# Optimization experiments

Hardware: AMD Instinct MI355X
Metric: run time of the kernel (lower is better)

The kernel has to match this reference:

```python
import jax, jax.numpy as jnp
import numpy as np

D_MODEL = 1024
NUM_HEADS = 16
HEAD_DIM = D_MODEL // NUM_HEADS
FF_DIM = 4096
EPS = 1e-5


def _layer_norm(x, gamma, beta):
    mu = jnp.mean(x, axis=-1, keepdims=True)
    var = jnp.var(x, axis=-1, keepdims=True)
    return (x - mu) * jax.lax.rsqrt(var + EPS) * gamma + beta


def setup_inputs() -> dict:
    key0 = jax.random.key(0)
    ks = jax.random.split(key0, 20)
    s = 0.02
    B, S = 2, 2048
    inp = {
        'value': jax.random.normal(ks[0], (B, S, D_MODEL), jnp.float32),
        'key': jax.random.normal(ks[1], (B, S, D_MODEL), jnp.float32),
        'query': jax.random.normal(ks[2], (B, S, D_MODEL), jnp.float32),
        # attention projections (stored [in, out]; y = x @ W + b)
        'wq': jax.random.normal(ks[3], (D_MODEL, D_MODEL), jnp.float32) * s,
        'bq': jnp.zeros((D_MODEL,), jnp.float32),
        'wk': jax.random.normal(ks[4], (D_MODEL, D_MODEL), jnp.float32) * s,
        'bk': jnp.zeros((D_MODEL,), jnp.float32),
        'wv': jax.random.normal(ks[5], (D_MODEL, D_MODEL), jnp.float32) * s,
        'bv': jnp.zeros((D_MODEL,), jnp.float32),
        'wo': jax.random.normal(ks[6], (D_MODEL, D_MODEL), jnp.float32) * s,
        'bo': jnp.zeros((D_MODEL,), jnp.float32),
        # layernorm 1
        'g1': jnp.ones((D_MODEL,), jnp.float32),
        'beta1': jnp.zeros((D_MODEL,), jnp.float32),
        # feed-forward
        'w1': jax.random.normal(ks[7], (D_MODEL, FF_DIM), jnp.float32) * s,
        'b1': jnp.zeros((FF_DIM,), jnp.float32),
        'w2': jax.random.normal(ks[8], (FF_DIM, D_MODEL), jnp.float32) * s,
        'b2': jnp.zeros((D_MODEL,), jnp.float32),
        # layernorm 2
        'g2': jnp.ones((D_MODEL,), jnp.float32),
        'beta2': jnp.zeros((D_MODEL,), jnp.float32),
    }
    return inp


def reference(value, key, query, wq, bq, wk, bk, wv, bv, wo, bo,
              g1, beta1, w1, b1, w2, b2, g2, beta2):
    B, S, _ = query.shape
    # QKV projections -> [B, S, H, Dh]
    Q = (query @ wq + bq).reshape(B, S, NUM_HEADS, HEAD_DIM)
    K = (key @ wk + bk).reshape(B, S, NUM_HEADS, HEAD_DIM)
    V = (value @ wv + bv).reshape(B, S, NUM_HEADS, HEAD_DIM)
    # scaled dot-product attention (full score matrix, as in source)
    energy = jnp.einsum('bqhd,bkhd->bhqk', Q, K) / jnp.sqrt(jnp.float32(HEAD_DIM))
    attn = jax.nn.softmax(energy, axis=-1)
    out = jnp.einsum('bhqk,bkhd->bqhd', attn, V).reshape(B, S, D_MODEL)
    attn_out = out @ wo + bo
    # residual + norm1 (dropout is identity in eval)
    x = _layer_norm(attn_out + query, g1, beta1)
    # feed-forward
    ff = jax.nn.relu(x @ w1 + b1) @ w2 + b2
    # residual + norm2
    return _layer_norm(ff + x, g2, beta2)
```

## Files before the change

kernel.cpp:

```cpp
#include <hip/hip_runtime.h>
#include <hip/hip_bf16.h>
#include <cstdint>
#include <math.h>

typedef __bf16 bf16_t;
typedef __attribute__((ext_vector_type(2))) __bf16 bf16x2;
typedef __attribute__((ext_vector_type(4))) __bf16 bf16x4;
typedef __attribute__((ext_vector_type(8))) __bf16 bf16x8;
typedef __attribute__((ext_vector_type(4))) float f32x4;
typedef __attribute__((ext_vector_type(16))) float f32x16;
typedef __attribute__((ext_vector_type(2))) int int2v;
typedef __attribute__((ext_vector_type(4))) int int4v;

#define B_SZ 2
#define S_SZ 2048
#define D_MODEL 1024
#define NUM_HEADS 16
#define HEAD_DIM 64
#define FF_DIM 4096
#define M_ROWS (B_SZ * S_SZ)

#define CF 0.180336880f
#define THRC 2.0f

__device__ __forceinline__ float fexp2(float x) { return __builtin_amdgcn_exp2f(x); }

__device__ __forceinline__ void gload_lds16(const void* g, void* lds) {
    __builtin_amdgcn_global_load_lds(
        (const __attribute__((address_space(1))) void*)(uintptr_t)g,
        (__attribute__((address_space(3))) void*)(uint32_t)(uintptr_t)lds,
        16, 0, 0);
}

__device__ __forceinline__ f32x4 mfma16(bf16x8 a, bf16x8 b, f32x4 c) {
    return __builtin_amdgcn_mfma_f32_16x16x32_bf16(a, b, c, 0, 0, 0);
}
__device__ __forceinline__ f32x16 mfma32(bf16x8 a, bf16x8 b, f32x16 c) {
    return __builtin_amdgcn_mfma_f32_32x32x16_bf16(a, b, c, 0, 0, 0);
}
__device__ __forceinline__ int2v plswap(int a, int b) {
    return __builtin_amdgcn_permlane32_swap(a, b, false, false);
}
__device__ __forceinline__ int packbf(float a, float b) {
    bf16x2 t; t[0] = (bf16_t)a; t[1] = (bf16_t)b;
    return __builtin_bit_cast(int, t);
}

__device__ __forceinline__ int xcd_swz(int lin, int nwg) {
    return (lin & 7) * (nwg >> 3) + (lin >> 3);
}

__global__ __launch_bounds__(256) void cast3_f32_bf16(const float* __restrict__ in0,
                                                      const float* __restrict__ in1,
                                                      const float* __restrict__ in2,
                                                      bf16_t* __restrict__ out0,
                                                      bf16_t* __restrict__ out1,
                                                      bf16_t* __restrict__ out2) {
    int which = blockIdx.x >> 12;
    int blk = blockIdx.x & 4095;
    const float* in = which == 0 ? in0 : which == 1 ? in1 : in2;
    bf16_t* out = which == 0 ? out0 : which == 1 ? out1 : out2;
    size_t i = ((size_t)blk * 256 + threadIdx.x) * 4;
    float4 v = *(const float4*)(in + i);
    bf16x4 o;
    o[0] = (bf16_t)v.x; o[1] = (bf16_t)v.y; o[2] = (bf16_t)v.z; o[3] = (bf16_t)v.w;
    *(bf16x4*)(out + i) = o;
}

__global__ __launch_bounds__(256) void transpose_cast_w4(const float* __restrict__ W0,
                                                         const float* __restrict__ W1,
                                                         const float* __restrict__ W2,
                                                         const float* __restrict__ W3,
                                                         bf16_t* __restrict__ T0,
                                                         bf16_t* __restrict__ T1,
                                                         bf16_t* __restrict__ T2,
                                                         bf16_t* __restrict__ T3) {
    __shared__ float t[32][33];
    const int K = 1024, N = 1024;
    const float* W = blockIdx.z == 0 ? W0 : blockIdx.z == 1 ? W1 : blockIdx.z == 2 ? W2 : W3;
    bf16_t* WT = blockIdx.z == 0 ? T0 : blockIdx.z == 1 ? T1 : blockIdx.z == 2 ? T2 : T3;
    int tid = threadIdx.x;
    int rr = tid >> 3, cc = (tid & 7) * 4;
    int k0 = blockIdx.x * 32, n0 = blockIdx.y * 32;
    float4 v = *(const float4*)(W + (size_t)(k0 + rr) * N + n0 + cc);
    t[rr][cc + 0] = v.x; t[rr][cc + 1] = v.y; t[rr][cc + 2] = v.z; t[rr][cc + 3] = v.w;
    __syncthreads();
    bf16x4 o;
    o[0] = (bf16_t)t[cc + 0][rr]; o[1] = (bf16_t)t[cc + 1][rr];
    o[2] = (bf16_t)t[cc + 2][rr]; o[3] = (bf16_t)t[cc + 3][rr];
    *(bf16x4*)(WT + (size_t)(n0 + rr) * K + k0 + cc) = o;
}

__global__ __launch_bounds__(256) void transpose_cast_w(const float* __restrict__ W,
                                                        bf16_t* __restrict__ WT,
                                                        int K, int N) {
    __shared__ float t[32][33];
    int tid = threadIdx.x;
    int rr = tid >> 3, cc = (tid & 7) * 4;
    int k0 = blockIdx.x * 32, n0 = blockIdx.y * 32;
    float4 v = *(const float4*)(W + (size_t)(k0 + rr) * N + n0 + cc);
    t[rr][cc + 0] = v.x; t[rr][cc + 1] = v.y; t[rr][cc + 2] = v.z; t[rr][cc + 3] = v.w;
    __syncthreads();
    bf16x4 o;
    o[0] = (bf16_t)t[cc + 0][rr]; o[1] = (bf16_t)t[cc + 1][rr];
    o[2] = (bf16_t)t[cc + 2][rr]; o[3] = (bf16_t)t[cc + 3][rr];
    *(bf16x4*)(WT + (size_t)(n0 + rr) * K + k0 + cc) = o;
}

__global__ __launch_bounds__(256) void transpose_v(const bf16_t* __restrict__ Vp,
                                                   bf16_t* __restrict__ VT) {
    __shared__ bf16_t t[32][34];
    int tid = threadIdx.x;
    int rr = tid >> 3, cc = (tid & 7) * 4;
    int bh = blockIdx.z;
    int b = bh >> 4, h = bh & 15;
    int s0 = blockIdx.x * 32, d0 = blockIdx.y * 32;
    bf16x4 v = *(const bf16x4*)(Vp + ((size_t)(b * S_SZ + s0 + rr)) * D_MODEL + h * HEAD_DIM + d0 + cc);
    t[rr][cc + 0] = v[0]; t[rr][cc + 1] = v[1]; t[rr][cc + 2] = v[2]; t[rr][cc + 3] = v[3];
    __syncthreads();
    bf16x4 o;
    o[0] = t[cc + 0][rr]; o[1] = t[cc + 1][rr]; o[2] = t[cc + 2][rr]; o[3] = t[cc + 3][rr];
    *(bf16x4*)(VT + ((size_t)(bh * HEAD_DIM + d0 + rr)) * S_SZ + s0 + cc) = o;
}

template<bool RELU, bool OUT_BF16, bool OUT_F32>
__device__ __forceinline__ void gemm_core(const bf16_t* __restrict__ A, int lda,
                                          const bf16_t* __restrict__ Bt, int ldb,
                                          const float* __restrict__ bias, bool useBias,
                                          float* __restrict__ Cf,
                                          bf16_t* __restrict__ Cb,
                                          int N, int Klen, int m0, int n0,
                                          bf16_t* sA, bf16_t* sB) {
    const int tid = threadIdx.x;
    const int lane = tid & 63, wave = tid >> 6;
    const int g = lane >> 4, r = lane & 15;
    const int wm = (wave >> 1) * 64, wn = (wave & 1) * 64;

    const bf16_t* Ablk = A + (size_t)m0 * lda;
    const bf16_t* Bblk = Bt + (size_t)n0 * ldb;
    const int c0 = wave * 64 + lane;
    const int c1 = c0 + 256;

    const bf16_t* a0 = Ablk + (size_t)(c0 >> 2) * lda + (c0 & 3) * 8;
    const bf16_t* a1 = Ablk + (size_t)(c1 >> 2) * lda + (c1 & 3) * 8;
    const bf16_t* b0 = Bblk + (size_t)(c0 >> 2) * ldb + (c0 & 3) * 8;
    const bf16_t* b1 = Bblk + (size_t)(c1 >> 2) * ldb + (c1 & 3) * 8;

    f32x4 acc[4][4];
#pragma unroll
    for (int i = 0; i < 4; i++)
#pragma unroll
        for (int j = 0; j < 4; j++)
#pragma unroll
            for (int e = 0; e < 4; e++) acc[i][j][e] = 0.f;

    auto stage = [&](int buf, int k0) {
        gload_lds16(a0 + k0, sA + buf * 4096 + wave * 512);
        gload_lds16(a1 + k0, sA + buf * 4096 + 2048 + wave * 512);
        gload_lds16(b0 + k0, sB + buf * 4096 + wave * 512);
        gload_lds16(b1 + k0, sB + buf * 4096 + 2048 + wave * 512);
    };
    auto compute = [&](int buf) {
        bf16x8 a[4], b[4];
#pragma unroll
        for (int i = 0; i < 4; i++)
            a[i] = *(const bf16x8*)(sA + buf * 4096 + (wm + i * 16 + r) * 32 + g * 8);
#pragma unroll
        for (int j = 0; j < 4; j++)
            b[j] = *(const bf16x8*)(sB + buf * 4096 + (wn + j * 16 + r) * 32 + g * 8);
#pragma unroll
        for (int i = 0; i < 4; i++)
#pragma unroll
            for (int j = 0; j < 4; j++)
                acc[i][j] = mfma16(a[i], b[j], acc[i][j]);
    };

    const int nk = Klen >> 5;
    stage(0, 0);
    stage(1, 32);
    int bc = 0, bs = 2;
    for (int s = 0; s < nk; ++s) {
        if (s + 2 < nk) {
            stage(bs, (s + 2) * 32);
            asm volatile("s_waitcnt vmcnt(8)" ::: "memory");
        } else if (s + 1 < nk) {
            asm volatile("s_waitcnt vmcnt(4)" ::: "memory");
        } else {
            asm volatile("s_waitcnt vmcnt(0)" ::: "memory");
        }
        __builtin_amdgcn_s_barrier();
        __builtin_amdgcn_sched_barrier(0);
        compute(bc);
        __builtin_amdgcn_sched_barrier(0);
        __builtin_amdgcn_s_barrier();
        bc = (bc + 1 == 3) ? 0 : bc + 1;
        bs = (bs + 1 == 3) ? 0 : bs + 1;
    }

#pragma unroll
    for (int j = 0; j < 4; j++) {
        int n = n0 + wn + j * 16 + r;
        float bv = useBias ? bias[n] : 0.f;
#pragma unroll
        for (int i = 0; i < 4; i++) {
#pragma unroll
            for (int rr = 0; rr < 4; rr++) {
                int mrow = m0 + wm + i * 16 + g * 4 + rr;
                float val = acc[i][j][rr] + bv;
                if (RELU) val = fmaxf(val, 0.f);
                if (OUT_F32) Cf[(size_t)mrow * N + n] = val;
                if (OUT_BF16) Cb[(size_t)mrow * N + n] = (bf16_t)val;
            }
        }
    }
}

template<bool RELU, bool OUT_BF16, bool OUT_F32>
__global__ __launch_bounds__(256) void gemm_bt(const bf16_t* __restrict__ A, int lda,
                                               const bf16_t* __restrict__ Bt, int ldb,
                                               const float* __restrict__ bias,
                                               float* __restrict__ Cf0,
                                               float* __restrict__ Cf1,
                                               bf16_t* __restrict__ Cb,
                                               int N, int Klen) {
    __shared__ bf16_t sA[3 * 4096];
    __shared__ bf16_t sB[3 * 4096];
    const int lin = blockIdx.x + gridDim.x * (blockIdx.y + gridDim.y * blockIdx.z);
    const int nwg = gridDim.x * gridDim.y * gridDim.z;
    const int swz = xcd_swz(lin, nwg);
    const int bx = swz % gridDim.x;
    const int rest = swz / gridDim.x;
    const int by = rest % gridDim.y;
    const int bz = rest / gridDim.y;
    const int koff = bz * Klen;
    gemm_core<RELU, OUT_BF16, OUT_F32>(A + koff, lda, Bt + koff, ldb, bias, bz == 0,
                                       bz ? Cf1 : Cf0, Cb, N, Klen, bx * 128, by * 128, sA, sB);
}

__global__ __launch_bounds__(256) void gemm_qkv(const bf16_t* __restrict__ A0,
                                                const bf16_t* __restrict__ A1,
                                                const bf16_t* __restrict__ A2,
                                                const bf16_t* __restrict__ B0,
                                                const bf16_t* __restrict__ B1,
                                                const bf16_t* __restrict__ B2,
                                                const float* __restrict__ b0,
                                                const float* __restrict__ b1,
                                                const float* __restrict__ b2,
                                                bf16_t* __restrict__ C0,
                                                bf16_t* __restrict__ C1,
                                                bf16_t* __restrict__ C2) {
    __shared__ bf16_t sA[3 * 4096];
    __shared__ bf16_t sB[3 * 4096];
    const int lin = blockIdx.x + gridDim.x * (blockIdx.y + gridDim.y * blockIdx.z);
    const int nwg = gridDim.x * gridDim.y * gridDim.z;
    const int swz = xcd_swz(lin, nwg);
    const int bx = swz % gridDim.x;
    const int rest = swz / gridDim.x;
    const int by = rest % gridDim.y;
    const int bz = rest / gridDim.y;
    const bf16_t* A = bz == 0 ? A0 : bz == 1 ? A1 : A2;
    const bf16_t* Bt = bz == 0 ? B0 : bz == 1 ? B1 : B2;
    const float* bias = bz == 0 ? b0 : bz == 1 ? b1 : b2;
    bf16_t* C = bz == 0 ? C0 : bz == 1 ? C1 : C2;
    gemm_core<false, true, false>(A, 1024, Bt, 1024, bias, true,
                                  nullptr, C, 1024, 1024, bx * 128, by * 128, sA, sB);
}

__device__ __forceinline__ void flash_tile(
    const char* kt, const char* vt, int l31, int hi,
    const bf16x8 (&bq)[4],
    f32x16& o0, f32x16& o1, float& mC, float& l_run)
{
    bf16x8 ak[4];
#pragma unroll
    for (int kb = 0; kb < 4; kb++)
        ak[kb] = *(const bf16x8*)(kt + l31 * 128 + (((kb << 1) | hi) ^ (l31 & 7)) * 16);
    bf16x8 av[4];
#pragma unroll
    for (int db = 0; db < 2; db++)
#pragma unroll
        for (int kb = 0; kb < 2; kb++)
            av[db * 2 + kb] = *(const bf16x8*)(vt + (db * 32 + l31) * 64 + ((((kb << 1) | hi)) ^ ((l31 >> 1) & 3)) * 16);

    f32x16 s;
#pragma unroll
    for (int e = 0; e < 16; e++) s[e] = 0.f;
#pragma unroll
    for (int kb = 0; kb < 4; kb++) s = mfma32(ak[kb], bq[kb], s);

    float ma = fmaxf(fmaxf(s[0], s[1]), fmaxf(s[2], s[3]));
    float mb = fmaxf(fmaxf(s[4], s[5]), fmaxf(s[6], s[7]));
    float mc = fmaxf(fmaxf(s[8], s[9]), fmaxf(s[10], s[11]));
    float md = fmaxf(fmaxf(s[12], s[13]), fmaxf(s[14], s[15]));
    float pmaxC = fmaxf(fmaxf(ma, mb), fmaxf(mc, md)) * CF;

    if (!__all(pmaxC <= mC + THRC)) {
        int2v pr = plswap(__float_as_int(pmaxC), __float_as_int(pmaxC));
        float rowmaxC = fmaxf(__int_as_float(pr[0]), __int_as_float(pr[1]));
        float mnewC = fmaxf(mC, rowmaxC);
        float alpha = fexp2(mC - mnewC);
        mC = mnewC;
        l_run *= alpha;
#pragma unroll
        for (int e = 0; e < 16; e++) { o0[e] *= alpha; o1[e] *= alpha; }
    }

#pragma unroll
    for (int e = 0; e < 16; e++) s[e] = fexp2(__builtin_fmaf(s[e], CF, -mC));
    float t0 = (s[0] + s[1]) + (s[2] + s[3]);
    float t1 = (s[4] + s[5]) + (s[6] + s[7]);
    float t2 = (s[8] + s[9]) + (s[10] + s[11]);
    float t3 = (s[12] + s[13]) + (s[14] + s[15]);
    l_run += (t0 + t1) + (t2 + t3);

#pragma unroll
    for (int kb2 = 0; kb2 < 2; kb2++) {
        const int bse = kb2 * 8;
        int W0 = packbf(s[bse + 0], s[bse + 1]);
        int W1 = packbf(s[bse + 2], s[bse + 3]);
        int W2 = packbf(s[bse + 4], s[bse + 5]);
        int W3 = packbf(s[bse + 6], s[bse + 7]);
        int2v r02 = plswap(W0, W2);
        int2v r13 = plswap(W1, W3);
        int4v fw; fw[0] = r02[0]; fw[1] = r13[0]; fw[2] = r02[1]; fw[3] = r13[1];
        bf16x8 pf = __builtin_bit_cast(bf16x8, fw);
        o0 = mfma32(av[kb2], pf, o0);
        o1 = mfma32(av[2 + kb2], pf, o1);
    }
}

__global__ __launch_bounds__(256) void flash_attn(const bf16_t* __restrict__ Qp,
                                                  const bf16_t* __restrict__ Kp,
                                                  const bf16_t* __restrict__ VT,
                                                  bf16_t* __restrict__ Oa) {
    __shared__ alignas(16) char lds[2][2][8192];
    const int tid = threadIdx.x;
    const int lane = tid & 63;
    const int wave = tid >> 6;
    const int half = wave >> 1;
    const int qt = wave & 1;
    const int l31 = lane & 31, hi = lane >> 5;

    const int lin = blockIdx.x + (blockIdx.y << 5) + (blockIdx.z << 9);
    const int swz = (lin & 7) * 128 + (lin >> 3);
    const int qb = swz & 31;
    const int h = (swz >> 5) & 15;
    const int b = swz >> 9;

    const int q0 = qb * 64 + qt * 32;

    const bf16_t* Qb = Qp + (size_t)b * S_SZ * D_MODEL + h * HEAD_DIM;
    const bf16_t* Kb = Kp + (size_t)b * S_SZ * D_MODEL + h * HEAD_DIM;
    const bf16_t* Vb = VT + ((size_t)(b * NUM_HEADS + h) * HEAD_DIM) * S_SZ;

    const int sh = wave & 1;
    const int skvbase = sh * (S_SZ / 2);
    const bool kRole = wave < 2;

    const bf16_t* src_run;
    size_t inner_stride;
    size_t tile_stride;
    char* dst0;
    char* dst1;
    if (kRole) {
        src_run = Kb + (size_t)(skvbase + (lane >> 3)) * D_MODEL + ((lane & 7) ^ (lane >> 3)) * 8;
        inner_stride = (size_t)8 * D_MODEL;
        tile_stride = (size_t)32 * D_MODEL;
        dst0 = &lds[0][sh][0] + lane * 16;
        dst1 = &lds[1][sh][0] + lane * 16;
    } else {
        src_run = Vb + (size_t)(lane >> 2) * S_SZ + skvbase + ((lane & 3) ^ ((lane >> 3) & 3)) * 8;
        inner_stride = (size_t)16 * S_SZ;
        tile_stride = 32;
        dst0 = &lds[0][sh][4096] + lane * 16;
        dst1 = &lds[1][sh][4096] + lane * 16;
    }

    bf16x8 bq[4];
#pragma unroll
    for (int kb = 0; kb < 4; kb++)
        bq[kb] = *(const bf16x8*)(Qb + (size_t)(q0 + l31) * D_MODEL + kb * 16 + hi * 8);

    f32x16 o0, o1;
#pragma unroll
    for (int e = 0; e < 16; e++) { o0[e] = 0.f; o1[e] = 0.f; }
    float mC = -1e30f, l_run = 0.f;

    const char* kt0 = &lds[0][half][0];
    const char* vt0 = &lds[0][half][4096];
    const char* kt1 = &lds[1][half][0];
    const char* vt1 = &lds[1][half][4096];

#pragma unroll
    for (int ii = 0; ii < 4; ii++)
        gload_lds16(src_run + ii * inner_stride, dst0 + ii * 1024);
    src_run += tile_stride;
    __syncthreads();

    for (int t = 0; t < 32; t += 2) {
#pragma unroll
        for (int ii = 0; ii < 4; ii++)
            gload_lds16(src_run + ii * inner_stride, dst1 + ii * 1024);
        src_run += tile_stride;
        flash_tile(kt0, vt0, l31, hi, bq, o0, o1, mC, l_run);
        __syncthreads();

        if (t + 2 < 32) {
#pragma unroll
            for (int ii = 0; ii < 4; ii++)
                gload_lds16(src_run + ii * inner_stride, dst0 + ii * 1024);
            src_run += tile_stride;
        }
        flash_tile(kt1, vt1, l31, hi, bq, o0, o1, mC, l_run);
        __syncthreads();
    }

    int2v lp = plswap(__float_as_int(l_run), __float_as_int(l_run));
    l_run = __int_as_float(lp[0]) + __int_as_float(lp[1]);

    float (*obuf)[2][64] = (float (*)[2][64])(&lds[0][0][0]);
    float (*mrg)[64][2] = (float (*)[64][2])(&lds[0][0][0] + 16384);
    if (half == 1) {
        mrg[qt][lane][0] = mC;
        mrg[qt][lane][1] = l_run;
#pragma unroll
        for (int e = 0; e < 16; e++) {
            obuf[e][qt][lane] = o0[e];
            obuf[16 + e][qt][lane] = o1[e];
        }
    }
    __syncthreads();
    if (half == 0) {
        const float m2C = mrg[qt][lane][0], l2 = mrg[qt][lane][1];
        const float mm = fmaxf(mC, m2C);
        const float e1 = fexp2(mC - mm);
        const float e2 = fexp2(m2C - mm);
        const float linv = 1.f / (l_run * e1 + l2 * e2);
        bf16_t* Orow = Oa + ((size_t)b * S_SZ + q0 + l31) * D_MODEL + h * HEAD_DIM;
#pragma unroll
        for (int db = 0; db < 2; db++) {
#pragma unroll
            for (int rq = 0; rq < 4; rq++) {
                bf16x4 st;
#pragma unroll
                for (int i = 0; i < 4; i++) {
                    const int e = rq * 4 + i;
                    const float own = db ? o1[e] : o0[e];
                    const float oth = obuf[db * 16 + e][qt][lane];
                    st[i] = (bf16_t)((own * e1 + oth * e2) * linv);
                }
                *(bf16x4*)(Orow + db * 32 + rq * 8 + hi * 4) = st;
            }
        }
    }
}

__global__ __launch_bounds__(256) void ln_fused(const float* __restrict__ A,
                                                const float* __restrict__ A2,
                                                const float* __restrict__ R,
                                                const float* __restrict__ gamma,
                                                const float* __restrict__ beta,
                                                float* __restrict__ Xf,
                                                bf16_t* __restrict__ Xb) {
    __shared__ float red[8];
    int row = blockIdx.x, tid = threadIdx.x;
    size_t base = (size_t)row * D_MODEL + tid * 4;
    float4 a = *(const float4*)(A + base);
    float4 rv = *(const float4*)(R + base);
    float v0 = a.x + rv.x, v1 = a.y + rv.y, v2 = a.z + rv.z, v3 = a.w + rv.w;
    if (A2) {
        float4 a2 = *(const float4*)(A2 + base);
        v0 += a2.x; v1 += a2.y; v2 += a2.z; v3 += a2.w;
    }
    float s = v0 + v1 + v2 + v3;
    float q = v0 * v0 + v1 * v1 + v2 * v2 + v3 * v3;
#pragma unroll
    for (int off = 32; off; off >>= 1) { s += __shfl_down(s, off); q += __shfl_down(q, off); }
    if ((tid & 63) == 0) { red[tid >> 6] = s; red[4 + (tid >> 6)] = q; }
    __syncthreads();
    s = red[0] + red[1] + red[2] + red[3];
    q = red[4] + red[5] + red[6] + red[7];
    float mean = s * (1.f / D_MODEL);
    float var = q * (1.f / D_MODEL) - mean * mean;
    float rstd = rsqrtf(var + 1e-5f);
    float4 gm = *(const float4*)(gamma + tid * 4);
    float4 bt = *(const float4*)(beta + tid * 4);
    float y0 = (v0 - mean) * rstd * gm.x + bt.x;
    float y1 = (v1 - mean) * rstd * gm.y + bt.y;
    float y2 = (v2 - mean) * rstd * gm.z + bt.z;
    float y3 = (v3 - mean) * rstd * gm.w + bt.w;
    float4 yo; yo.x = y0; yo.y = y1; yo.z = y2; yo.w = y3;
    *(float4*)(Xf + base) = yo;
    if (Xb) {
        bf16x4 ob; ob[0] = (bf16_t)y0; ob[1] = (bf16_t)y1; ob[2] = (bf16_t)y2; ob[3] = (bf16_t)y3;
        *(bf16x4*)(Xb + base) = ob;
    }
}

extern "C" void kernel_launch(void* const* d_in, const int* in_sizes, int n_in,
                              void* d_out, int out_size, void* d_ws, size_t ws_size,
                              hipStream_t stream) {
    const float* value = (const float*)d_in[0];
    const float* key   = (const float*)d_in[1];
    const float* query = (const float*)d_in[2];
    const float* wq = (const float*)d_in[3];
    const float* bq = (const float*)d_in[4];
    const float* wk = (const float*)d_in[5];
    const float* bk = (const float*)d_in[6];
    const float* wv = (const float*)d_in[7];
    const float* bv = (const float*)d_in[8];
    const float* wo = (const float*)d_in[9];
    const float* bo = (const float*)d_in[10];
    const float* g1 = (const float*)d_in[11];
    const float* beta1 = (const float*)d_in[12];
    const float* w1 = (const float*)d_in[13];
    const float* b1 = (const float*)d_in[14];
    const float* w2 = (const float*)d_in[15];
    const float* b2 = (const float*)d_in[16];
    const float* g2 = (const float*)d_in[17];
    const float* beta2 = (const float*)d_in[18];
    (void)in_sizes; (void)n_in; (void)out_size; (void)ws_size;

    const size_t MB = 1ull << 20;
    char* ws = (char*)d_ws;
    bf16_t* wqT = (bf16_t*)(ws + 0 * MB);
    bf16_t* wkT = (bf16_t*)(ws + 2 * MB);
    bf16_t* wvT = (bf16_t*)(ws + 4 * MB);
    bf16_t* woT = (bf16_t*)(ws + 6 * MB);
    bf16_t* w1T = (bf16_t*)(ws + 8 * MB);
    bf16_t* w2T = (bf16_t*)(ws + 16 * MB);
    bf16_t* q_bf = (bf16_t*)(ws + 24 * MB);
    bf16_t* k_bf = (bf16_t*)(ws + 32 * MB);
    bf16_t* v_bf = (bf16_t*)(ws + 40 * MB);
    bf16_t* Qp  = (bf16_t*)(ws + 48 * MB);
    bf16_t* Kp  = (bf16_t*)(ws + 56 * MB);
    bf16_t* Vp  = (bf16_t*)(ws + 64 * MB);
    bf16_t* VT  = (bf16_t*)(ws + 72 * MB);
    bf16_t* attn = (bf16_t*)(ws + 24 * MB);
    float*  woP0 = (float*)(ws + 32 * MB);
    float*  woP1 = (float*)(ws + 48 * MB);
    float*  x_f = (float*)(ws + 64 * MB);
    bf16_t* x_b = (bf16_t*)(ws + 24 * MB);
    bf16_t* h_b = (bf16_t*)(ws + 32 * MB);
    float*  ffP0 = (float*)(ws + 80 * MB);
    float*  ffP1 = (float*)(ws + 96 * MB);

    dim3 blk(256);

    cast3_f32_bf16<<<12288, blk, 0, stream>>>(query, key, value, q_bf, k_bf, v_bf);
    transpose_cast_w4<<<dim3(32, 32, 4), blk, 0, stream>>>(wq, wk, wv, wo, wqT, wkT, wvT, woT);
    transpose_cast_w<<<dim3(32, 128), blk, 0, stream>>>(w1, w1T, 1024, 4096);
    transpose_cast_w<<<dim3(128, 32), blk, 0, stream>>>(w2, w2T, 4096, 1024);

    gemm_qkv<<<dim3(32, 8, 3), blk, 0, stream>>>(q_bf, k_bf, v_bf, wqT, wkT, wvT,
                                                 bq, bk, bv, Qp, Kp, Vp);

    transpose_v<<<dim3(64, 2, 32), blk, 0, stream>>>(Vp, VT);

    flash_attn<<<dim3(32, 16, 2), blk, 0, stream>>>(Qp, Kp, VT, attn);

    gemm_bt<false, false, true><<<dim3(32, 8, 2), blk, 0, stream>>>(attn, 1024, woT, 1024, bo, woP0, woP1, nullptr, D_MODEL, 512);

    ln_fused<<<4096, blk, 0, stream>>>(woP0, woP1, query, g1, beta1, x_f, x_b);

    gemm_bt<true, true, false><<<dim3(32, 32, 1), blk, 0, stream>>>(x_b, 1024, w1T, 1024, b1, nullptr, nullptr, h_b, FF_DIM, 1024);

    gemm_bt<false, false, true><<<dim3(32, 8, 2), blk, 0, stream>>>(h_b, 4096, w2T, 4096, b2, ffP0, ffP1, nullptr, D_MODEL, 2048);

    ln_fused<<<4096, blk, 0, stream>>>(ffP0, ffP1, x_f, g2, beta2, (float*)d_out, nullptr);
}
```

Baseline: 263.6 us.

## Enlarge GEMM tiles to 256-row blocks with 512-thread workgroups

Replaces the 128x128 GEMM core with a 256xN tile (N=256 or 128) run by 8 waves per workgroup, each wave computing a 128x(16*BNF) sub-tile. The aim is more data reuse per LDS load and fewer global loads per MFMA across the QKV, output-projection and FFN GEMMs. In exchange, LDS use and accumulator registers go up and there are fewer workgroups. The 2-way split-K GEMMs now launch only 256 blocks, which risks poor load balance across CUs.

After: 259.7 us. Within noise of the previous version (-1.5%).

```diff
diff --git a/kernel.cpp b/kernel.cpp
--- a/kernel.cpp
+++ b/kernel.cpp
@@ -123,55 +123,55 @@
     *(bf16x4*)(VT + ((size_t)(bh * HEAD_DIM + d0 + rr)) * S_SZ + s0 + cc) = o;
 }
 
-template<bool RELU, bool OUT_BF16, bool OUT_F32>
-__device__ __forceinline__ void gemm_core(const bf16_t* __restrict__ A, int lda,
-                                          const bf16_t* __restrict__ Bt, int ldb,
-                                          const float* __restrict__ bias, bool useBias,
-                                          float* __restrict__ Cf,
-                                          bf16_t* __restrict__ Cb,
-                                          int N, int Klen, int m0, int n0,
-                                          bf16_t* sA, bf16_t* sB) {
+template<int BNF, bool RELU, bool OUT_BF16, bool OUT_F32>
+__device__ __forceinline__ void gemm_core256(const bf16_t* __restrict__ A, int lda,
+                                             const bf16_t* __restrict__ Bt, int ldb,
+                                             const float* __restrict__ bias, bool useBias,
+                                             float* __restrict__ Cf,
+                                             bf16_t* __restrict__ Cb,
+                                             int N, int Klen, int m0, int n0,
+                                             bf16_t* sA, bf16_t* sB) {
     const int tid = threadIdx.x;
-    const int lane = tid & 63, wave = tid >> 6;
+    const int lane = tid & 63, w = tid >> 6;
     const int g = lane >> 4, r = lane & 15;
-    const int wm = (wave >> 1) * 64, wn = (wave & 1) * 64;
+    const int wm = (w >> 2) * 128;
+    const int wn = (w & 3) * (16 * BNF);
+    const int ABUF = 8192;
+    const int BBUF = (BNF == 4) ? 8192 : 4096;
 
     const bf16_t* Ablk = A + (size_t)m0 * lda;
     const bf16_t* Bblk = Bt + (size_t)n0 * ldb;
-    const int c0 = wave * 64 + lane;
-    const int c1 = c0 + 256;
-
-    const bf16_t* a0 = Ablk + (size_t)(c0 >> 2) * lda + (c0 & 3) * 8;
-    const bf16_t* a1 = Ablk + (size_t)(c1 >> 2) * lda + (c1 & 3) * 8;
-    const bf16_t* b0 = Bblk + (size_t)(c0 >> 2) * ldb + (c0 & 3) * 8;
-    const bf16_t* b1 = Bblk + (size_t)(c1 >> 2) * ldb + (c1 & 3) * 8;
-
-    f32x4 acc[4][4];
-#pragma unroll
-    for (int i = 0; i < 4; i++)
-#pragma unroll
-        for (int j = 0; j < 4; j++)
+    const bf16_t* a0 = Ablk + (size_t)(tid >> 2) * lda + (tid & 3) * 8;
+    const bf16_t* a1 = a0 + (size_t)128 * lda;
+    const bf16_t* b0 = Bblk + (size_t)(tid >> 2) * ldb + (tid & 3) * 8;
+    const bf16_t* b1 = b0 + (size_t)128 * ldb;
+
+    f32x4 acc[8][BNF];
+#pragma unroll
+    for (int i = 0; i < 8; i++)
+#pragma unroll
+        for (int j = 0; j < BNF; j++)
 #pragma unroll
             for (int e = 0; e < 4; e++) acc[i][j][e] = 0.f;
 
     auto stage = [&](int buf, int k0) {
-        gload_lds16(a0 + k0, sA + buf * 4096 + wave * 512);
-        gload_lds16(a1 + k0, sA + buf * 4096 + 2048 + wave * 512);
-        gload_lds16(b0 + k0, sB + buf * 4096 + wave * 512);
-        gload_lds16(b1 + k0, sB + buf * 4096 + 2048 + wave * 512);
+        gload_lds16(a0 + k0, sA + buf * ABUF + tid * 8);
+        gload_lds16(a1 + k0, sA + buf * ABUF + 4096 + tid * 8);
+        gload_lds16(b0 + k0, sB + buf * BBUF + tid * 8);
+        if (BNF == 4) gload_lds16(b1 + k0, sB + buf * BBUF + 4096 + tid * 8);
     };
     auto compute = [&](int buf) {
-        bf16x8 a[4], b[4];
-#pragma unroll
-        for (int i = 0; i < 4; i++)
-            a[i] = *(const bf16x8*)(sA + buf * 4096 + (wm + i * 16 + r) * 32 + g * 8);
-#pragma unroll
-        for (int j = 0; j < 4; j++)
-            b[j] = *(const bf16x8*)(sB + buf * 4096 + (wn + j * 16 + r) * 32 + g * 8);
-#pragma unroll
-        for (int i = 0; i < 4; i++)
-#pragma unroll
-            for (int j = 0; j < 4; j++)
+        bf16x8 a[8], b[BNF];
+#pragma unroll
+        for (int i = 0; i < 8; i++)
+            a[i] = *(const bf16x8*)(sA + buf * ABUF + (wm + i * 16 + r) * 32 + g * 8);
+#pragma unroll
+        for (int j = 0; j < BNF; j++)
+            b[j] = *(const bf16x8*)(sB + buf * BBUF + (wn + j * 16 + r) * 32 + g * 8);
+#pragma unroll
+        for (int i = 0; i < 8; i++)
+#pragma unroll
+            for (int j = 0; j < BNF; j++)
                 acc[i][j] = mfma16(a[i], b[j], acc[i][j]);
     };
 
@@ -182,9 +182,11 @@
     for (int s = 0; s < nk; ++s) {
         if (s + 2 < nk) {
             stage(bs, (s + 2) * 32);
-            asm volatile("s_waitcnt vmcnt(8)" ::: "memory");
+            if (BNF == 4) asm volatile("s_waitcnt vmcnt(8)" ::: "memory");
+            else          asm volatile("s_waitcnt vmcnt(6)" ::: "memory");
         } else if (s + 1 < nk) {
-            asm volatile("s_waitcnt vmcnt(4)" ::: "memory");
+            if (BNF == 4) asm volatile("s_waitcnt vmcnt(4)" ::: "memory");
+            else          asm volatile("s_waitcnt vmcnt(3)" ::: "memory");
         } else {
             asm volatile("s_waitcnt vmcnt(0)" ::: "memory");
         }
@@ -198,11 +200,11 @@
     }
 
 #pragma unroll
-    for (int j = 0; j < 4; j++) {
+    for (int j = 0; j < BNF; j++) {
         int n = n0 + wn + j * 16 + r;
         float bv = useBias ? bias[n] : 0.f;
 #pragma unroll
-        for (int i = 0; i < 4; i++) {
+        for (int i = 0; i < 8; i++) {
 #pragma unroll
             for (int rr = 0; rr < 4; rr++) {
                 int mrow = m0 + wm + i * 16 + g * 4 + rr;
@@ -215,16 +217,16 @@
     }
 }
 
-template<bool RELU, bool OUT_BF16, bool OUT_F32>
-__global__ __launch_bounds__(256) void gemm_bt(const bf16_t* __restrict__ A, int lda,
-                                               const bf16_t* __restrict__ Bt, int ldb,
-                                               const float* __restrict__ bias,
-                                               float* __restrict__ Cf0,
-                                               float* __restrict__ Cf1,
-                                               bf16_t* __restrict__ Cb,
-                                               int N, int Klen) {
-    __shared__ bf16_t sA[3 * 4096];
-    __shared__ bf16_t sB[3 * 4096];
+template<int BNF, bool RELU, bool OUT_BF16, bool OUT_F32>
+__global__ __launch_bounds__(512, 2) void gemm_bt256(const bf16_t* __restrict__ A, int lda,
+                                                     const bf16_t* __restrict__ Bt, int ldb,
+                                                     const float* __restrict__ bias,
+                                                     float* __restrict__ Cf0,
+                                                     float* __restrict__ Cf1,
+                                                     bf16_t* __restrict__ Cb,
+                                                     int N, int Klen) {
+    __shared__ bf16_t sA[3 * 8192];
+    __shared__ bf16_t sB[3 * ((BNF == 4) ? 8192 : 4096)];
     const int lin = blockIdx.x + gridDim.x * (blockIdx.y + gridDim.y * blockIdx.z);
     const int nwg = gridDim.x * gridDim.y * gridDim.z;
     const int swz = xcd_swz(lin, nwg);
@@ -233,24 +235,25 @@
     const int by = rest % gridDim.y;
     const int bz = rest / gridDim.y;
     const int koff = bz * Klen;
-    gemm_core<RELU, OUT_BF16, OUT_F32>(A + koff, lda, Bt + koff, ldb, bias, bz == 0,
-                                       bz ? Cf1 : Cf0, Cb, N, Klen, bx * 128, by * 128, sA, sB);
-}
-
-__global__ __launch_bounds__(256) void gemm_qkv(const bf16_t* __restrict__ A0,
-                                                const bf16_t* __restrict__ A1,
-                                                const bf16_t* __restrict__ A2,
-                                                const bf16_t* __restrict__ B0,
-                                                const bf16_t* __restrict__ B1,
-                                                const bf16_t* __restrict__ B2,
-                                                const float* __restrict__ b0,
-                                                const float* __restrict__ b1,
-                                                const float* __restrict__ b2,
-                                                bf16_t* __restrict__ C0,
-                                                bf16_t* __restrict__ C1,
-                                                bf16_t* __restrict__ C2) {
-    __shared__ bf16_t sA[3 * 4096];
-    __shared__ bf16_t sB[3 * 4096];
+    gemm_core256<BNF, RELU, OUT_BF16, OUT_F32>(A + koff, lda, Bt + koff, ldb, bias, bz == 0,
+                                               bz ? Cf1 : Cf0, Cb, N, Klen,
+                                               bx * 256, by * (64 * BNF), sA, sB);
+}
+
+__global__ __launch_bounds__(512, 2) void gemm_qkv256(const bf16_t* __restrict__ A0,
+                                                      const bf16_t* __restrict__ A1,
+                                                      const bf16_t* __restrict__ A2,
+                                                      const bf16_t* __restrict__ B0,
+                                                      const bf16_t* __restrict__ B1,
+                                                      const bf16_t* __restrict__ B2,
+                                                      const float* __restrict__ b0,
+                                                      const float* __restrict__ b1,
+                                                      const float* __restrict__ b2,
+                                                      bf16_t* __restrict__ C0,
+                                                      bf16_t* __restrict__ C1,
+                                                      bf16_t* __restrict__ C2) {
+    __shared__ bf16_t sA[3 * 8192];
+    __shared__ bf16_t sB[3 * 8192];
     const int lin = blockIdx.x + gridDim.x * (blockIdx.y + gridDim.y * blockIdx.z);
     const int nwg = gridDim.x * gridDim.y * gridDim.z;
     const int swz = xcd_swz(lin, nwg);
@@ -262,8 +265,8 @@
     const bf16_t* Bt = bz == 0 ? B0 : bz == 1 ? B1 : B2;
     const float* bias = bz == 0 ? b0 : bz == 1 ? b1 : b2;
     bf16_t* C = bz == 0 ? C0 : bz == 1 ? C1 : C2;
-    gemm_core<false, true, false>(A, 1024, Bt, 1024, bias, true,
-                                  nullptr, C, 1024, 1024, bx * 128, by * 128, sA, sB);
+    gemm_core256<4, false, true, false>(A, 1024, Bt, 1024, bias, true,
+                                        nullptr, C, 1024, 1024, bx * 256, by * 256, sA, sB);
 }
 
 __device__ __forceinline__ void flash_tile(
@@ -546,26 +549,27 @@
     float*  ffP1 = (float*)(ws + 96 * MB);
 
     dim3 blk(256);
+    dim3 blk512(512);
 
     cast3_f32_bf16<<<12288, blk, 0, stream>>>(query, key, value, q_bf, k_bf, v_bf);
     transpose_cast_w4<<<dim3(32, 32, 4), blk, 0, stream>>>(wq, wk, wv, wo, wqT, wkT, wvT, woT);
     transpose_cast_w<<<dim3(32, 128), blk, 0, stream>>>(w1, w1T, 1024, 4096);
     transpose_cast_w<<<dim3(128, 32), blk, 0, stream>>>(w2, w2T, 4096, 1024);
 
-    gemm_qkv<<<dim3(32, 8, 3), blk, 0, stream>>>(q_bf, k_bf, v_bf, wqT, wkT, wvT,
-                                                 bq, bk, bv, Qp, Kp, Vp);
+    gemm_qkv256<<<dim3(16, 4, 3), blk512, 0, stream>>>(q_bf, k_bf, v_bf, wqT, wkT, wvT,
+                                                       bq, bk, bv, Qp, Kp, Vp);
 
     transpose_v<<<dim3(64, 2, 32), blk, 0, stream>>>(Vp, VT);
 
     flash_attn<<<dim3(32, 16, 2), blk, 0, stream>>>(Qp, Kp, VT, attn);
 
-    gemm_bt<false, false, true><<<dim3(32, 8, 2), blk, 0, stream>>>(attn, 1024, woT, 1024, bo, woP0, woP1, nullptr, D_MODEL, 512);
+    gemm_bt256<2, false, false, true><<<dim3(16, 8, 2), blk512, 0, stream>>>(attn, 1024, woT, 1024, bo, woP0, woP1, nullptr, D_MODEL, 512);
 
     ln_fused<<<4096, blk, 0, stream>>>(woP0, woP1, query, g1, beta1, x_f, x_b);
 
-    gemm_bt<true, true, false><<<dim3(32, 32, 1), blk, 0, stream>>>(x_b, 1024, w1T, 1024, b1, nullptr, nullptr, h_b, FF_DIM, 1024);
-
-    gemm_bt<false, false, true><<<dim3(32, 8, 2), blk, 0, stream>>>(h_b, 4096, w2T, 4096, b2, ffP0, ffP1, nullptr, D_MODEL, 2048);
+    gemm_bt256<4, true, true, false><<<dim3(16, 16, 1), blk512, 0, stream>>>(x_b, 1024, w1T, 1024, b1, nullptr, nullptr, h_b, FF_DIM, 1024);
+
+    gemm_bt256<2, false, false, true><<<dim3(16, 8, 2), blk512, 0, stream>>>(h_b, 4096, w2T, 4096, b2, ffP0, ffP1, nullptr, D_MODEL, 2048);
 
     ln_fused<<<4096, blk, 0, stream>>>(ffP0, ffP1, x_f, g2, beta2, (float*)d_out, nullptr);
 }
```
